# Kernel optimization log

Hardware: AMD Instinct MI355X
Metric: run time of the kernel (lower is better)

The kernel has to match this reference:

```python
import jax, jax.numpy as jnp
import numpy as np


NUM_HEADS = 16


def setup_inputs() -> dict:
    key = jax.random.key(0)
    ks = jax.random.split(key, 6)
    B, Sq, Skv, DQ, DKV = 2, 1024, 4096, 1024, 768
    return {
        "x_q": jax.random.normal(ks[0], (B, Sq, DQ), jnp.float32),
        "x_kv": jax.random.normal(ks[1], (B, Skv, DKV), jnp.float32),
        "Wq": jax.random.normal(ks[2], (DQ, DQ), jnp.float32) * 0.02,
        "Wk": jax.random.normal(ks[3], (DQ, DKV), jnp.float32) * 0.02,
        "Wv": jax.random.normal(ks[4], (DQ, DKV), jnp.float32) * 0.02,
        "Wo": jax.random.normal(ks[5], (DQ, DQ), jnp.float32) * 0.02,
    }


def _split_heads(x):
    # Faithful to torch view(B, H, S, hd): a pure reshape, NOT a transpose.
    B, S, D = x.shape
    return x.reshape(B, NUM_HEADS, S, D // NUM_HEADS)


def reference(x_q, x_kv, Wq, Wk, Wv, Wo):
    head_dim = x_q.shape[-1] // NUM_HEADS
    # torch Linear: y = x @ W.T, weight shape (out, in)
    Q = _split_heads(jnp.einsum("bsd,od->bso", x_q, Wq))   # (B,H,Sq',hd)
    K = _split_heads(jnp.einsum("bsd,od->bso", x_kv, Wk))  # (B,H,Skv',hd)
    V = _split_heads(jnp.einsum("bsd,od->bso", x_kv, Wv))
    # Scale is 1/head_dim (not 1/sqrt), faithful to the source.
    scores = jnp.einsum("bhqd,bhkd->bhqk", Q, K) / head_dim
    attn = jax.nn.softmax(scores, axis=-1)
    out = jnp.einsum("bhqk,bhkd->bhqd", attn, V)  # (B,H,Sq',hd)
    B, Sq, DQ = x_q.shape
    out = out.transpose(0, 2, 1, 3).reshape(B, Sq, DQ)
    return jnp.einsum("bsd,od->bso", out, Wo)
```

## Files before the change

### kernel.cpp

```cpp
#include <hip/hip_runtime.h>
#include <hip/hip_bf16.h>
#include <cstdint>

#define THREADS 256

typedef __attribute__((ext_vector_type(8))) short bf16x8;
typedef __attribute__((ext_vector_type(4))) float f32x4;

__device__ __forceinline__ void load_lds16(const void* g, void* l) {
    __builtin_amdgcn_global_load_lds(
        (const __attribute__((address_space(1))) unsigned int*)g,
        (__attribute__((address_space(3))) unsigned int*)l, 16, 0, 0);
}

__device__ __forceinline__ unsigned short f2bf(float x) {
    __hip_bfloat16 hb = __float2bfloat16(x);
    return *(unsigned short*)&hb;
}

__global__ __launch_bounds__(THREADS)
void cast_inputs(const float* __restrict__ xq, const float* __restrict__ xkv,
                 const float* __restrict__ wq, const float* __restrict__ wk,
                 const float* __restrict__ wv, const float* __restrict__ wo,
                 unsigned short* __restrict__ oq, unsigned short* __restrict__ okv,
                 unsigned short* __restrict__ owq, unsigned short* __restrict__ owk,
                 unsigned short* __restrict__ owv, unsigned short* __restrict__ owo) {
    const unsigned n0 = 524288, n1 = 1572864, n2 = 262144, n3 = 196608, n4 = 196608;
    unsigned i = blockIdx.x * THREADS + threadIdx.x;
    const float* src; unsigned short* dst; unsigned off;
    if (i < n0)                    { src = xq;  dst = oq;  off = i; }
    else if (i < n0+n1)            { src = xkv; dst = okv; off = i - n0; }
    else if (i < n0+n1+n2)         { src = wq;  dst = owq; off = i - n0 - n1; }
    else if (i < n0+n1+n2+n3)      { src = wk;  dst = owk; off = i - n0 - n1 - n2; }
    else if (i < n0+n1+n2+n3+n4)   { src = wv;  dst = owv; off = i - n0 - n1 - n2 - n3; }
    else                           { src = wo;  dst = owo; off = i - n0 - n1 - n2 - n3 - n4; }
    float4 v = *(const float4*)(src + (size_t)off * 4);
    ushort4 o;
    o.x = f2bf(v.x); o.y = f2bf(v.y); o.z = f2bf(v.z); o.w = f2bf(v.w);
    *(ushort4*)(dst + (size_t)off * 4) = o;
}

__global__ __launch_bounds__(THREADS)
void gemm_proj(const unsigned short* __restrict__ xkv, const unsigned short* __restrict__ wkv,
               unsigned short* __restrict__ Kn, unsigned short* __restrict__ Vt,
               const unsigned short* __restrict__ xq, const unsigned short* __restrict__ wq,
               unsigned short* __restrict__ Qout) {
    __shared__ __align__(16) unsigned short As[128 * 64];
    __shared__ __align__(16) unsigned short Bs[128 * 64];

    const int t    = threadIdx.x;
    const int w    = t >> 6;
    const int lane = t & 63;
    const int l15  = lane & 15;
    const int quad = lane >> 4;
    const int wm   = w & 1;
    const int wn   = w >> 1;

    if (blockIdx.x < 1024) {
        const int bN = (blockIdx.x & 15) * 128;
        const int bM = (blockIdx.x >> 4) * 128;
        const int Kd = 768;

        const int srow = t >> 3;
        const int scol = ((t & 7) ^ ((t >> 4) & 7)) << 3;
        const unsigned short* ga = xkv + (size_t)(bM + srow) * Kd + scol;
        const unsigned short* gb = wkv + (size_t)(bN + srow) * Kd + scol;
        const int lbase = w * 512;

        const int xr = (l15 >> 1) & 7;
        int aoff[2][4], boff[2][4];
#pragma unroll
        for (int kk = 0; kk < 2; ++kk)
#pragma unroll
            for (int mt = 0; mt < 4; ++mt) {
                aoff[kk][mt] = (wm * 64 + mt * 16 + l15) * 64 + (((kk * 4 + quad) ^ xr) << 3);
                boff[kk][mt] = (wn * 64 + mt * 16 + l15) * 64 + (((kk * 4 + quad) ^ xr) << 3);
            }

        f32x4 acc[4][4];
#pragma unroll
        for (int mt = 0; mt < 4; ++mt)
#pragma unroll
            for (int nt = 0; nt < 4; ++nt)
#pragma unroll
                for (int r = 0; r < 4; ++r) acc[mt][nt][r] = 0.f;

        for (int k0 = 0; k0 < Kd; k0 += 64) {
            __syncthreads();
#pragma unroll
            for (int it = 0; it < 4; ++it) {
                load_lds16(ga + (size_t)it * 32 * Kd + k0, &As[lbase + it * 2048]);
                load_lds16(gb + (size_t)it * 32 * Kd + k0, &Bs[lbase + it * 2048]);
            }
            __syncthreads();

#pragma unroll
            for (int kk = 0; kk < 2; ++kk) {
                bf16x8 af[4], bf[4];
#pragma unroll
                for (int mt = 0; mt < 4; ++mt) af[mt] = *(const bf16x8*)&As[aoff[kk][mt]];
#pragma unroll
                for (int nt = 0; nt < 4; ++nt) bf[nt] = *(const bf16x8*)&Bs[boff[kk][nt]];
#pragma unroll
                for (int mt = 0; mt < 4; ++mt)
#pragma unroll
                    for (int nt = 0; nt < 4; ++nt)
                        acc[mt][nt] = __builtin_amdgcn_mfma_f32_16x16x32_bf16(af[mt], bf[nt], acc[mt][nt], 0, 0, 0);
            }
        }

        const int rbase = bM + wm * 64;
        const int b  = rbase >> 12;
        const int h  = (rbase & 4095) >> 8;
        if (bN < 1024) {
            const int G = (bN + wn * 64) >> 6;
            unsigned short* kp = Kn + (size_t)(b * 16 + h) * 262144 + (size_t)G * 256 * 64 + l15;
#pragma unroll
            for (int mt = 0; mt < 4; ++mt)
#pragma unroll
                for (int r = 0; r < 4; ++r) {
                    int u = (rbase & 255) + mt * 16 + quad * 4 + r;
                    unsigned short* cp = kp + (size_t)u * 64;
#pragma unroll
                    for (int nt = 0; nt < 4; ++nt) cp[nt * 16] = f2bf(acc[mt][nt][r]);
                }
        } else {
            const int Gv = (bN - 1024 + wn * 64) >> 6;
            unsigned short* vp = Vt + (size_t)(b * 16 + h) * 262144 + (size_t)Gv * 256;
#pragma unroll
            for (int nt = 0; nt < 4; ++nt) {
                int d = nt * 16 + l15;
#pragma unroll
                for (int mt = 0; mt < 4; ++mt) {
                    int u = (rbase & 255) + mt * 16 + quad * 4;
                    ushort4 pk;
                    pk.x = f2bf(acc[mt][nt][0]);
                    pk.y = f2bf(acc[mt][nt][1]);
                    pk.z = f2bf(acc[mt][nt][2]);
                    pk.w = f2bf(acc[mt][nt][3]);
                    *(ushort4*)(vp + (size_t)d * 4096 + u) = pk;
                }
            }
        }
    } else {
        const int id = blockIdx.x - 1024;
        const int bN = (id & 15) * 64;
        const int bM = (id >> 4) * 64;
        const int Kd = 1024, N = 1024;

        const int srow = t >> 3;
        const int scol = ((t & 7) ^ ((t >> 3) & 7)) << 3;
        const unsigned short* ga = xq + (size_t)(bM + srow) * Kd + scol;
        const unsigned short* gb = wq + (size_t)(bN + srow) * Kd + scol;
        const int lbase = w * 512;

        int aoff[2][2], boff[2][2];
#pragma unroll
        for (int kk = 0; kk < 2; ++kk)
#pragma unroll
            for (int mt = 0; mt < 2; ++mt) {
                aoff[kk][mt] = (wm * 32 + mt * 16 + l15) * 64 + (((kk * 4 + quad) ^ (l15 & 7)) << 3);
                boff[kk][mt] = (wn * 32 + mt * 16 + l15) * 64 + (((kk * 4 + quad) ^ (l15 & 7)) << 3);
            }

        f32x4 acc[2][2];
#pragma unroll
        for (int mt = 0; mt < 2; ++mt)
#pragma unroll
            for (int nt = 0; nt < 2; ++nt)
#pragma unroll
                for (int r = 0; r < 4; ++r) acc[mt][nt][r] = 0.f;

        for (int k0 = 0; k0 < Kd; k0 += 64) {
            __syncthreads();
#pragma unroll
            for (int it = 0; it < 2; ++it) {
                load_lds16(ga + (size_t)it * 32 * Kd + k0, &As[lbase + it * 2048]);
                load_lds16(gb + (size_t)it * 32 * Kd + k0, &Bs[lbase + it * 2048]);
            }
            __syncthreads();

#pragma unroll
            for (int kk = 0; kk < 2; ++kk) {
                bf16x8 af[2], bf[2];
#pragma unroll
                for (int mt = 0; mt < 2; ++mt) af[mt] = *(const bf16x8*)&As[aoff[kk][mt]];
#pragma unroll
                for (int nt = 0; nt < 2; ++nt) bf[nt] = *(const bf16x8*)&Bs[boff[kk][nt]];
#pragma unroll
                for (int mt = 0; mt < 2; ++mt)
#pragma unroll
                    for (int nt = 0; nt < 2; ++nt)
                        acc[mt][nt] = __builtin_amdgcn_mfma_f32_16x16x32_bf16(af[mt], bf[nt], acc[mt][nt], 0, 0, 0);
            }
        }

#pragma unroll
        for (int mt = 0; mt < 2; ++mt)
#pragma unroll
            for (int r = 0; r < 4; ++r) {
                int row = bM + wm * 32 + mt * 16 + quad * 4 + r;
                int col = bN + wn * 32 + l15;
                unsigned short* cp = Qout + (size_t)row * N + col;
#pragma unroll
                for (int nt = 0; nt < 2; ++nt) cp[nt * 16] = f2bf(acc[mt][nt][r]);
            }
    }
}

template <bool OUTF32>
__global__ __launch_bounds__(THREADS)
void gemm_bf16_nt64(const unsigned short* __restrict__ A, const unsigned short* __restrict__ W,
                    void* __restrict__ Cout, int M, int N, int Kd) {
    __shared__ __align__(16) unsigned short As[64 * 64];
    __shared__ __align__(16) unsigned short Bs[64 * 64];

    const int t    = threadIdx.x;
    const int w    = t >> 6;
    const int lane = t & 63;
    const int l15  = lane & 15;
    const int quad = lane >> 4;
    const int wm   = w & 1;
    const int wn   = w >> 1;
    const int bM = blockIdx.y * 64;
    const int bN = blockIdx.x * 64;

    const int srow = t >> 3;
    const int scol = ((t & 7) ^ ((t >> 3) & 7)) << 3;
    const unsigned short* ga = A + (size_t)(bM + srow) * Kd + scol;
    const unsigned short* gb = W + (size_t)(bN + srow) * Kd + scol;
    const int lbase = w * 512;

    int aoff[2][2], boff[2][2];
#pragma unroll
    for (int kk = 0; kk < 2; ++kk)
#pragma unroll
        for (int mt = 0; mt < 2; ++mt) {
            aoff[kk][mt] = (wm * 32 + mt * 16 + l15) * 64 + (((kk * 4 + quad) ^ (l15 & 7)) << 3);
            boff[kk][mt] = (wn * 32 + mt * 16 + l15) * 64 + (((kk * 4 + quad) ^ (l15 & 7)) << 3);
        }

    f32x4 acc[2][2];
#pragma unroll
    for (int mt = 0; mt < 2; ++mt)
#pragma unroll
        for (int nt = 0; nt < 2; ++nt)
#pragma unroll
            for (int r = 0; r < 4; ++r) acc[mt][nt][r] = 0.f;

    for (int k0 = 0; k0 < Kd; k0 += 64) {
        __syncthreads();
#pragma unroll
        for (int it = 0; it < 2; ++it) {
            load_lds16(ga + (size_t)it * 32 * Kd + k0, &As[lbase + it * 2048]);
            load_lds16(gb + (size_t)it * 32 * Kd + k0, &Bs[lbase + it * 2048]);
        }
        __syncthreads();

#pragma unroll
        for (int kk = 0; kk < 2; ++kk) {
            bf16x8 af[2], bf[2];
#pragma unroll
            for (int mt = 0; mt < 2; ++mt) af[mt] = *(const bf16x8*)&As[aoff[kk][mt]];
#pragma unroll
            for (int nt = 0; nt < 2; ++nt) bf[nt] = *(const bf16x8*)&Bs[boff[kk][nt]];
#pragma unroll
            for (int mt = 0; mt < 2; ++mt)
#pragma unroll
                for (int nt = 0; nt < 2; ++nt)
                    acc[mt][nt] = __builtin_amdgcn_mfma_f32_16x16x32_bf16(af[mt], bf[nt], acc[mt][nt], 0, 0, 0);
        }
    }

#pragma unroll
    for (int mt = 0; mt < 2; ++mt)
#pragma unroll
        for (int r = 0; r < 4; ++r) {
            int row = bM + wm * 32 + mt * 16 + quad * 4 + r;
            int col = bN + wn * 32 + l15;
            if (OUTF32) {
                float* cp = (float*)Cout + (size_t)row * N + col;
#pragma unroll
                for (int nt = 0; nt < 2; ++nt) cp[nt * 16] = acc[mt][nt][r];
            } else {
                unsigned short* cp = (unsigned short*)Cout + (size_t)row * N + col;
#pragma unroll
                for (int nt = 0; nt < 2; ++nt) cp[nt * 16] = f2bf(acc[mt][nt][r]);
            }
        }
}

__global__ __launch_bounds__(THREADS, 2)
void attn_mfma9(const unsigned short* __restrict__ Q, const unsigned short* __restrict__ K,
                const unsigned short* __restrict__ Vt, unsigned short* __restrict__ AO) {
    extern __shared__ __align__(16) unsigned short sm[];
    unsigned short* Ks = sm;
    unsigned short* Vs = sm + 8192;
    unsigned short* Ps = sm + 16384;
    float* OS = (float*)sm;
    float* Lw = (float*)(sm + 26624);

    const int bid  = blockIdx.x;
    const int slot = bid >> 3;
    const int qq   = slot & 15;
    const int hh   = (bid & 7) + 8 * (slot >> 4);
    const int q0 = qq * 64;
    const int h  = hh & 15;
    const int b  = hh >> 4;

    const int t    = threadIdx.x;
    const int w    = t >> 6;
    const int lane = t & 63;
    const int l15  = lane & 15;
    const int quad = lane >> 4;

    const unsigned short* Qh = Q + (size_t)b * 1048576 + (size_t)h * 65536 + (size_t)q0 * 64;
    const unsigned short* Kh = K + (size_t)b * 4194304 + (size_t)h * 262144;
    const unsigned short* Vh = Vt + (size_t)(b * 16 + h) * 262144;

    bf16x8 Qb[4][2];
#pragma unroll
    for (int qt = 0; qt < 4; ++qt)
#pragma unroll
        for (int kk = 0; kk < 2; ++kk)
            Qb[qt][kk] = *(const bf16x8*)(Qh + (size_t)(qt * 16 + l15) * 64 + kk * 32 + quad * 8);

    const unsigned short* gKw = Kh + (size_t)(w * 32 + (lane >> 3)) * 64
                                   + (((lane & 7) ^ ((lane >> 3) & 7)) << 3);
    const unsigned short* gVw = Vh + (size_t)(lane >> 2) * 4096 + w * 32
                                   + (((lane & 3) ^ ((lane >> 2) & 3)) << 3);
    const int ldsK = w * 2048;
    const int ldsV = w * 2048;

    int koff[2][2];
#pragma unroll
    for (int kvt = 0; kvt < 2; ++kvt)
#pragma unroll
        for (int kk = 0; kk < 2; ++kk)
            koff[kvt][kk] = (w * 32 + kvt * 16 + l15) * 64 + (((kk * 4 + quad) ^ (l15 & 7)) << 3);
    int voff[4];
#pragma unroll
    for (int dt = 0; dt < 4; ++dt)
        voff[dt] = w * 2048 + (dt * 16 + l15) * 32 + ((quad ^ (l15 & 3)) << 3);

    const int pw  = w * 2560;
    const int pq  = pw + l15 * 40;

    f32x4 Oacc[4][4];
#pragma unroll
    for (int qt = 0; qt < 4; ++qt)
#pragma unroll
        for (int dt = 0; dt < 4; ++dt)
#pragma unroll
            for (int r = 0; r < 4; ++r) Oacc[qt][dt][r] = 0.f;
    float lsum[4] = {0.f, 0.f, 0.f, 0.f};

    const float scale = 1.0f / 64.0f;

#pragma unroll
    for (int it = 0; it < 4; ++it)
        load_lds16(gKw + it * 512, &Ks[ldsK + it * 512]);
#pragma unroll
    for (int it = 0; it < 4; ++it)
        load_lds16(gVw + (size_t)it * 65536, &Vs[ldsV + it * 512]);

    for (int kc = 0; kc < 32; ++kc) {
        const int kn = (kc + 1) & 31;

        asm volatile("s_waitcnt vmcnt(4)" ::: "memory");

        bf16x8 ka0 = *(const bf16x8*)&Ks[koff[0][0]];
        bf16x8 kb0 = *(const bf16x8*)&Ks[koff[0][1]];
        bf16x8 ka1 = *(const bf16x8*)&Ks[koff[1][0]];
        bf16x8 kb1 = *(const bf16x8*)&Ks[koff[1][1]];
        asm volatile("s_waitcnt lgkmcnt(0)" ::: "memory");
#pragma unroll
        for (int it = 0; it < 4; ++it)
            load_lds16(gKw + (size_t)kn * 8192 + it * 512, &Ks[ldsK + it * 512]);

#pragma unroll
        for (int qt = 0; qt < 4; ++qt) {
            f32x4 S0 = {0.f, 0.f, 0.f, 0.f};
            S0 = __builtin_amdgcn_mfma_f32_16x16x32_bf16(ka0, Qb[qt][0], S0, 0, 0, 0);
            S0 = __builtin_amdgcn_mfma_f32_16x16x32_bf16(kb0, Qb[qt][1], S0, 0, 0, 0);
            f32x4 S1 = {0.f, 0.f, 0.f, 0.f};
            S1 = __builtin_amdgcn_mfma_f32_16x16x32_bf16(ka1, Qb[qt][0], S1, 0, 0, 0);
            S1 = __builtin_amdgcn_mfma_f32_16x16x32_bf16(kb1, Qb[qt][1], S1, 0, 0, 0);
            float p0 = __expf(S0[0] * scale);
            float p1 = __expf(S0[1] * scale);
            float p2 = __expf(S0[2] * scale);
            float p3 = __expf(S0[3] * scale);
            float p4 = __expf(S1[0] * scale);
            float p5 = __expf(S1[1] * scale);
            float p6 = __expf(S1[2] * scale);
            float p7 = __expf(S1[3] * scale);
            lsum[qt] += ((p0 + p1) + (p2 + p3)) + ((p4 + p5) + (p6 + p7));
            ushort4 pk4a, pk4b;
            pk4a.x = f2bf(p0); pk4a.y = f2bf(p1); pk4a.z = f2bf(p2); pk4a.w = f2bf(p3);
            pk4b.x = f2bf(p4); pk4b.y = f2bf(p5); pk4b.z = f2bf(p6); pk4b.w = f2bf(p7);
            *(ushort4*)&Ps[pq + qt * 640 + quad * 4]      = pk4a;
            *(ushort4*)&Ps[pq + qt * 640 + 16 + quad * 4] = pk4b;
        }

        asm volatile("s_waitcnt vmcnt(4)" ::: "memory");
        asm volatile("s_waitcnt lgkmcnt(0)" ::: "memory");

        bf16x8 Vf[4], Pa[4];
#pragma unroll
        for (int dt = 0; dt < 4; ++dt) Vf[dt] = *(const bf16x8*)&Vs[voff[dt]];
#pragma unroll
        for (int qt = 0; qt < 4; ++qt) Pa[qt] = *(const bf16x8*)&Ps[pq + qt * 640 + quad * 8];
        asm volatile("s_waitcnt lgkmcnt(0)" ::: "memory");
#pragma unroll
        for (int it = 0; it < 4; ++it)
            load_lds16(gVw + (size_t)kn * 128 + (size_t)it * 65536, &Vs[ldsV + it * 512]);

#pragma unroll
        for (int qt = 0; qt < 4; ++qt)
#pragma unroll
            for (int dt = 0; dt < 4; ++dt)
                Oacc[qt][dt] = __builtin_amdgcn_mfma_f32_16x16x32_bf16(Pa[qt], Vf[dt], Oacc[qt][dt], 0, 0, 0);
    }

#pragma unroll
    for (int qt = 0; qt < 4; ++qt) {
        float v = lsum[qt];
        v += __shfl_xor(v, 16);
        v += __shfl_xor(v, 32);
        lsum[qt] = v;
    }
    __syncthreads();
    if (lane < 16) {
#pragma unroll
        for (int qt = 0; qt < 4; ++qt)
            Lw[w * 64 + qt * 16 + lane] = lsum[qt];
    }
    if (w > 0) {
        float* myOS = OS + (w - 1) * 4352;
#pragma unroll
        for (int qt = 0; qt < 4; ++qt)
#pragma unroll
            for (int dt = 0; dt < 4; ++dt)
                *(f32x4*)&myOS[(dt * 16 + l15) * 68 + qt * 16 + quad * 4] = Oacc[qt][dt];
    }
    __syncthreads();
    if (w == 0) {
#pragma unroll
        for (int qt = 0; qt < 4; ++qt) {
            f32x4 lv = *(const f32x4*)&Lw[qt * 16 + quad * 4];
            lv += *(const f32x4*)&Lw[64 + qt * 16 + quad * 4];
            lv += *(const f32x4*)&Lw[128 + qt * 16 + quad * 4];
            lv += *(const f32x4*)&Lw[192 + qt * 16 + quad * 4];
            f32x4 inv;
#pragma unroll
            for (int r = 0; r < 4; ++r) inv[r] = 1.0f / lv[r];
#pragma unroll
            for (int dt = 0; dt < 4; ++dt) {
                f32x4 o = Oacc[qt][dt];
                int os = (dt * 16 + l15) * 68 + qt * 16 + quad * 4;
                o += *(const f32x4*)&OS[os];
                o += *(const f32x4*)&OS[4352 + os];
                o += *(const f32x4*)&OS[8704 + os];
#pragma unroll
                for (int r = 0; r < 4; ++r) {
                    int q = qt * 16 + quad * 4 + r;
                    AO[(size_t)b * 1048576 + (size_t)(q0 + q) * 1024 + (h << 6) + dt * 16 + l15]
                        = f2bf(o[r] * inv[r]);
                }
            }
        }
    }
}

extern "C" void kernel_launch(void* const* d_in, const int* in_sizes, int n_in,
                              void* d_out, int out_size, void* d_ws, size_t ws_size,
                              hipStream_t stream) {
    const float* x_q  = (const float*)d_in[0];
    const float* x_kv = (const float*)d_in[1];
    const float* Wq   = (const float*)d_in[2];
    const float* Wk   = (const float*)d_in[3];
    const float* Wv   = (const float*)d_in[4];
    const float* Wo   = (const float*)d_in[5];
    float* out = (float*)d_out;

    unsigned short* base   = (unsigned short*)d_ws;
    unsigned short* xq_bf  = base;
    unsigned short* xkv_bf = base + 2097152;
    unsigned short* wq_bf  = base + 8388608;
    unsigned short* wk_bf  = base + 9437184;
    unsigned short* wv_bf  = base + 10223616;
    unsigned short* wo_bf  = base + 11010048;
    unsigned short* Qw     = base + 12058624;
    unsigned short* Kw     = base + 14155776;
    unsigned short* AOb    = base + 22544384;
    unsigned short* Vtw    = base + 30932992;

    dim3 blk(THREADS);
    cast_inputs<<<dim3(11776), blk, 0, stream>>>(x_q, x_kv, Wq, Wk, Wv, Wo,
                                                 xq_bf, xkv_bf, wq_bf, wk_bf, wv_bf, wo_bf);
    gemm_proj<<<dim3(1536), blk, 0, stream>>>(xkv_bf, wk_bf, Kw, Vtw, xq_bf, wq_bf, Qw);
    attn_mfma9<<<dim3(512), blk, 54272, stream>>>(Qw, Kw, Vtw, AOb);
    gemm_bf16_nt64<true><<<dim3(16, 32), blk, 0, stream>>>(AOb, wo_bf, (void*)out, 2048, 1024, 1024);
}
```

Measured before the change: 198.7 us.

## Keep attention probabilities in registers via lane permutes instead of LDS round-trip

The attention kernel no longer writes the bf16 probability tile P to shared memory and reads it back in MFMA A-operand layout. Instead it packs pairs with v_cvt_pk_bf16, then rearranges them across lanes with permlane32_swap and a xor-16 shuffle. It also replaces __expf(x/64) with a native exp2 on a prescaled argument, and raises wave priority around the PV MFMA block. This removes LDS stores, loads and one wait per KV chunk, at the cost of extra cross-lane permute instructions and some added register pressure.

```diff
diff --git a/kernel.cpp b/kernel.cpp
--- a/kernel.cpp
+++ b/kernel.cpp
@@ -6,6 +6,7 @@
 
 typedef __attribute__((ext_vector_type(8))) short bf16x8;
 typedef __attribute__((ext_vector_type(4))) float f32x4;
+typedef __attribute__((ext_vector_type(2))) unsigned int u32x2;
 
 __device__ __forceinline__ void load_lds16(const void* g, void* l) {
     __builtin_amdgcn_global_load_lds(
@@ -16,6 +17,34 @@
 __device__ __forceinline__ unsigned short f2bf(float x) {
     __hip_bfloat16 hb = __float2bfloat16(x);
     return *(unsigned short*)&hb;
+}
+
+__device__ __forceinline__ unsigned cvt_pk_bf16(float lo, float hi) {
+    unsigned r;
+    asm("v_cvt_pk_bf16_f32 %0, %1, %2" : "=v"(r) : "v"(lo), "v"(hi));
+    return r;
+}
+
+__device__ __forceinline__ float fexp2(float x) {
+#if __has_builtin(__builtin_amdgcn_exp2f)
+    return __builtin_amdgcn_exp2f(x);
+#else
+    return exp2f(x);
+#endif
+}
+
+__device__ __forceinline__ void swap32(unsigned& lo, unsigned& hi) {
+#if __has_builtin(__builtin_amdgcn_permlane32_swap)
+    u32x2 r = __builtin_amdgcn_permlane32_swap(lo, hi, false, false);
+    lo = r[0]; hi = r[1];
+#else
+    unsigned plo = (unsigned)__shfl_xor((int)lo, 32, 64);
+    unsigned phi = (unsigned)__shfl_xor((int)hi, 32, 64);
+    bool up = (threadIdx.x & 32) != 0;
+    unsigned nlo = up ? phi : lo;
+    unsigned nhi = up ? hi : plo;
+    lo = nlo; hi = nhi;
+#endif
 }
 
 __global__ __launch_bounds__(THREADS)
@@ -291,12 +320,11 @@
 }
 
 __global__ __launch_bounds__(THREADS, 2)
-void attn_mfma9(const unsigned short* __restrict__ Q, const unsigned short* __restrict__ K,
-                const unsigned short* __restrict__ Vt, unsigned short* __restrict__ AO) {
+void attn_mfma10(const unsigned short* __restrict__ Q, const unsigned short* __restrict__ K,
+                 const unsigned short* __restrict__ Vt, unsigned short* __restrict__ AO) {
     extern __shared__ __align__(16) unsigned short sm[];
     unsigned short* Ks = sm;
     unsigned short* Vs = sm + 8192;
-    unsigned short* Ps = sm + 16384;
     float* OS = (float*)sm;
     float* Lw = (float*)(sm + 26624);
 
@@ -313,6 +341,7 @@
     const int lane = t & 63;
     const int l15  = lane & 15;
     const int quad = lane >> 4;
+    const int qsel = quad & 1;
 
     const unsigned short* Qh = Q + (size_t)b * 1048576 + (size_t)h * 65536 + (size_t)q0 * 64;
     const unsigned short* Kh = K + (size_t)b * 4194304 + (size_t)h * 262144;
@@ -343,9 +372,6 @@
     for (int dt = 0; dt < 4; ++dt)
         voff[dt] = w * 2048 + (dt * 16 + l15) * 32 + ((quad ^ (l15 & 3)) << 3);
 
-    const int pw  = w * 2560;
-    const int pq  = pw + l15 * 40;
-
     f32x4 Oacc[4][4];
 #pragma unroll
     for (int qt = 0; qt < 4; ++qt)
@@ -355,7 +381,7 @@
             for (int r = 0; r < 4; ++r) Oacc[qt][dt][r] = 0.f;
     float lsum[4] = {0.f, 0.f, 0.f, 0.f};
 
-    const float scale = 1.0f / 64.0f;
+    const float e2s = 0.022542110013890053f;
 
 #pragma unroll
     for (int it = 0; it < 4; ++it)
@@ -378,6 +404,7 @@
         for (int it = 0; it < 4; ++it)
             load_lds16(gKw + (size_t)kn * 8192 + it * 512, &Ks[ldsK + it * 512]);
 
+        bf16x8 Pa[4];
 #pragma unroll
         for (int qt = 0; qt < 4; ++qt) {
             f32x4 S0 = {0.f, 0.f, 0.f, 0.f};
@@ -386,40 +413,48 @@
             f32x4 S1 = {0.f, 0.f, 0.f, 0.f};
             S1 = __builtin_amdgcn_mfma_f32_16x16x32_bf16(ka1, Qb[qt][0], S1, 0, 0, 0);
             S1 = __builtin_amdgcn_mfma_f32_16x16x32_bf16(kb1, Qb[qt][1], S1, 0, 0, 0);
-            float p0 = __expf(S0[0] * scale);
-            float p1 = __expf(S0[1] * scale);
-            float p2 = __expf(S0[2] * scale);
-            float p3 = __expf(S0[3] * scale);
-            float p4 = __expf(S1[0] * scale);
-            float p5 = __expf(S1[1] * scale);
-            float p6 = __expf(S1[2] * scale);
-            float p7 = __expf(S1[3] * scale);
+            float p0 = fexp2(S0[0] * e2s);
+            float p1 = fexp2(S0[1] * e2s);
+            float p2 = fexp2(S0[2] * e2s);
+            float p3 = fexp2(S0[3] * e2s);
+            float p4 = fexp2(S1[0] * e2s);
+            float p5 = fexp2(S1[1] * e2s);
+            float p6 = fexp2(S1[2] * e2s);
+            float p7 = fexp2(S1[3] * e2s);
             lsum[qt] += ((p0 + p1) + (p2 + p3)) + ((p4 + p5) + (p6 + p7));
-            ushort4 pk4a, pk4b;
-            pk4a.x = f2bf(p0); pk4a.y = f2bf(p1); pk4a.z = f2bf(p2); pk4a.w = f2bf(p3);
-            pk4b.x = f2bf(p4); pk4b.y = f2bf(p5); pk4b.z = f2bf(p6); pk4b.w = f2bf(p7);
-            *(ushort4*)&Ps[pq + qt * 640 + quad * 4]      = pk4a;
-            *(ushort4*)&Ps[pq + qt * 640 + 16 + quad * 4] = pk4b;
+            unsigned ca = cvt_pk_bf16(p0, p1);
+            unsigned cb = cvt_pk_bf16(p2, p3);
+            unsigned cc = cvt_pk_bf16(p4, p5);
+            unsigned cd = cvt_pk_bf16(p6, p7);
+            swap32(ca, cc);
+            swap32(cb, cd);
+            unsigned r0 = (unsigned)__shfl_xor((int)(qsel ? ca : cc), 16, 64);
+            unsigned r1 = (unsigned)__shfl_xor((int)(qsel ? cb : cd), 16, 64);
+            union { unsigned u[4]; bf16x8 v; } pk_;
+            pk_.u[0] = qsel ? r0 : ca;
+            pk_.u[1] = qsel ? r1 : cb;
+            pk_.u[2] = qsel ? cc : r0;
+            pk_.u[3] = qsel ? cd : r1;
+            Pa[qt] = pk_.v;
         }
 
         asm volatile("s_waitcnt vmcnt(4)" ::: "memory");
-        asm volatile("s_waitcnt lgkmcnt(0)" ::: "memory");
-
-        bf16x8 Vf[4], Pa[4];
+
+        bf16x8 Vf[4];
 #pragma unroll
         for (int dt = 0; dt < 4; ++dt) Vf[dt] = *(const bf16x8*)&Vs[voff[dt]];
-#pragma unroll
-        for (int qt = 0; qt < 4; ++qt) Pa[qt] = *(const bf16x8*)&Ps[pq + qt * 640 + quad * 8];
         asm volatile("s_waitcnt lgkmcnt(0)" ::: "memory");
 #pragma unroll
         for (int it = 0; it < 4; ++it)
             load_lds16(gVw + (size_t)kn * 128 + (size_t)it * 65536, &Vs[ldsV + it * 512]);
 
+        __builtin_amdgcn_s_setprio(1);
 #pragma unroll
         for (int qt = 0; qt < 4; ++qt)
 #pragma unroll
             for (int dt = 0; dt < 4; ++dt)
                 Oacc[qt][dt] = __builtin_amdgcn_mfma_f32_16x16x32_bf16(Pa[qt], Vf[dt], Oacc[qt][dt], 0, 0, 0);
+        __builtin_amdgcn_s_setprio(0);
     }
 
 #pragma unroll
@@ -499,6 +534,6 @@
     cast_inputs<<<dim3(11776), blk, 0, stream>>>(x_q, x_kv, Wq, Wk, Wv, Wo,
                                                  xq_bf, xkv_bf, wq_bf, wk_bf, wv_bf, wo_bf);
     gemm_proj<<<dim3(1536), blk, 0, stream>>>(xkv_bf, wk_bf, Kw, Vtw, xq_bf, wq_bf, Qw);
-    attn_mfma9<<<dim3(512), blk, 54272, stream>>>(Qw, Kw, Vtw, AOb);
+    attn_mfma10<<<dim3(512), blk, 54272, stream>>>(Qw, Kw, Vtw, AOb);
     gemm_bf16_nt64<true><<<dim3(16, 32), blk, 0, stream>>>(AOb, wo_bf, (void*)out, 2048, 1024, 1024);
 }
```

Measured after the change: 204.8 us. 1.03x slower.
